# Optimization experiments

Hardware: AMD Instinct MI355X
Metric: run time of the kernel (lower is better)

Reference implementation:

```python
import jax, jax.numpy as jnp
import numpy as np

IOU_THRESH = 0.5
NEG_POS_RATIO = 3
VAR0, VAR1 = 0.1, 0.2  # BoxCoder variances


def box_iou(a, b):
    # a: [G,4] xyxy, b: [P,4] xyxy -> [G,P]
    lt = jnp.maximum(a[:, None, :2], b[None, :, :2])
    rb = jnp.minimum(a[:, None, 2:], b[None, :, 2:])
    wh = jnp.clip(rb - lt, 0.0)
    inter = wh[..., 0] * wh[..., 1]
    area_a = (a[:, 2] - a[:, 0]) * (a[:, 3] - a[:, 1])
    area_b = (b[:, 2] - b[:, 0]) * (b[:, 3] - b[:, 1])
    return inter / (area_a[:, None] + area_b[None, :] - inter)


def xywha_to_xyxy(p):
    c, wh = p[:, :2], p[:, 2:]
    return jnp.concatenate([c - wh * 0.5, c + wh * 0.5], axis=-1)


def assign_targets(gt_boxes, gt_labels, priors_xyxy):
    # gt_boxes [G,4], gt_labels [G], priors_xyxy [P,4]
    iou = box_iou(gt_boxes, priors_xyxy)            # [G,P]
    matched_vals = iou.max(axis=0)                  # [P]
    matches = iou.argmax(axis=0)                    # [P]
    best_prior = iou.argmax(axis=1)                 # [G] best prior per target
    G = gt_boxes.shape[0]
    matches = matches.at[best_prior].set(jnp.arange(G))
    matched_vals = matched_vals.at[best_prior].set(2.0)
    labels = jnp.where(matched_vals < IOU_THRESH, 0, gt_labels[matches])  # [P]
    boxes = gt_boxes[matches]                       # [P,4]
    return boxes, labels


def encode(boxes_xyxy, priors_xywha):
    # SSD center-form encoding with variances
    ctr = (boxes_xyxy[:, :2] + boxes_xyxy[:, 2:]) * 0.5
    wh = boxes_xyxy[:, 2:] - boxes_xyxy[:, :2]
    g_c = (ctr - priors_xywha[:, :2]) / (VAR0 * priors_xywha[:, 2:])
    g_wh = jnp.log(wh / priors_xywha[:, 2:]) / VAR1
    return jnp.concatenate([g_c, g_wh], axis=-1)


def hard_negative_mask(bg_loss, labels):
    # bg_loss [B,P]: -log_softmax(logits)[...,0]; keep all positives and
    # top-(ratio*num_pos) hardest negatives per image.
    pos = labels > 0
    num_neg = pos.sum(axis=1, keepdims=True) * NEG_POS_RATIO
    loss = jnp.where(pos, -jnp.inf, bg_loss)
    order = jnp.argsort(-loss, axis=1)
    rank = jnp.argsort(order, axis=1)
    return pos | (rank < num_neg)


def reference(priors, class_logits, box_regression, gt_boxes, gt_labels):
    priors_xyxy = xywha_to_xyxy(priors)
    boxes, labels = jax.vmap(assign_targets, in_axes=(0, 0, None))(
        gt_boxes, gt_labels, priors_xyxy)            # [B,P,4], [B,P]
    regression_targets = jax.vmap(encode, in_axes=(0, None))(boxes, priors)

    logp = jax.nn.log_softmax(class_logits, axis=-1)  # [B,P,C]
    bg_loss = jax.lax.stop_gradient(-logp[..., 0])
    mask = hard_negative_mask(bg_loss, labels)        # [B,P] bool

    # masked cross-entropy, reduction='sum'
    ce = -jnp.take_along_axis(logp, labels[..., None], axis=-1)[..., 0]
    loss_classifier = jnp.sum(jnp.where(mask, ce, 0.0))

    # masked smooth-L1 (beta=1), reduction='sum' over positives
    pos = labels > 0
    d = jnp.abs(box_regression - regression_targets)
    sl1 = jnp.where(d < 1.0, 0.5 * d * d, d - 0.5)
    loss_box_reg = jnp.sum(jnp.where(pos[..., None], sl1, 0.0))

    num_pos = jnp.sum(pos).astype(class_logits.dtype)
    return loss_box_reg / num_pos, loss_classifier / num_pos


def setup_inputs() -> dict:
    key = jax.random.key(0)
    ks = jax.random.split(key, 8)
    B, P, C, G = 64, 8732, 81, 16
    # priors: xywha in [0,1] with small positive wh
    p_c = jax.random.uniform(ks[0], (P, 2), jnp.float32, 0.05, 0.95)
    p_wh = jax.random.uniform(ks[1], (P, 2), jnp.float32, 0.02, 0.25)
    priors = jnp.concatenate([p_c, p_wh], axis=-1)
    class_logits = jax.random.normal(ks[2], (B, P, C), jnp.float32)
    box_regression = jax.random.normal(ks[3], (B, P, 4), jnp.float32)
    # gt boxes: valid xyxy in [0,1] with positive size
    g_c = jax.random.uniform(ks[4], (B, G, 2), jnp.float32, 0.2, 0.8)
    g_wh = jax.random.uniform(ks[5], (B, G, 2), jnp.float32, 0.05, 0.3)
    gt_boxes = jnp.concatenate([g_c - g_wh * 0.5, g_c + g_wh * 0.5], axis=-1)
    gt_labels = jax.random.randint(ks[6], (B, G), 1, C, jnp.int32)
    return {"priors": priors, "class_logits": class_logits,
            "box_regression": box_regression, "gt_boxes": gt_boxes,
            "gt_labels": gt_labels}
```

## Files before the change

kernel.cpp:

```cpp
#include <hip/hip_runtime.h>
#include <cfloat>

#define GT 16
#define NCLS 81
#define TPB 256
#define MAXP 8732
#define TROWS 64
#define WF4 324
#define TF4 (TROWS*NCLS/4)

__device__ __forceinline__ float smoothl1(float d){
  float a = fabsf(d);
  return a < 1.0f ? 0.5f*a*a : a - 0.5f;
}

__global__ __launch_bounds__(TPB) void assign1(
    const float* __restrict__ priors,
    const float* __restrict__ gt_boxes,
    long long* __restrict__ best,
    float* __restrict__ mvv,
    unsigned char* __restrict__ mmatch,
    float* __restrict__ ce_pos, float* __restrict__ sl1_sum,
    int* __restrict__ num_pos, float* __restrict__ out,
    int P)
{
  const int b = blockIdx.x >> 3, chunk = blockIdx.x & 7;
  const int CH = (P + 7) >> 3;
  const int p0 = chunk*CH, p1 = min(p0 + CH, P);
  const int tid = threadIdx.x, wave = tid >> 6, lane = tid & 63;
  if (chunk == 0 && tid == 0){ ce_pos[b] = 0.0f; sl1_sum[b] = 0.0f; num_pos[b] = 0; }
  if (blockIdx.x == 0 && tid < 2) out[tid] = 0.0f;
  __shared__ float gx0[GT], gy0[GT], gx1[GT], gy1[GT], ga[GT];
  __shared__ float redv[4*GT]; __shared__ int redi[4*GT];
  if (tid < GT){
    const float4 gb = ((const float4*)gt_boxes)[b*GT + tid];
    gx0[tid]=gb.x; gy0[tid]=gb.y; gx1[tid]=gb.z; gy1[tid]=gb.w;
    ga[tid] = (gb.z-gb.x)*(gb.w-gb.y);
  }
  __syncthreads();
  float bv[GT]; int bi[GT];
  #pragma unroll
  for (int g=0; g<GT; ++g){ bv[g] = -1.0f; bi[g] = 0x7fffffff; }
  for (int p = p0 + tid; p < p1; p += TPB){
    const float4 pr = ((const float4*)priors)[p];
    const float px0 = pr.x - pr.z*0.5f, py0 = pr.y - pr.w*0.5f;
    const float px1 = pr.x + pr.z*0.5f, py1 = pr.y + pr.w*0.5f;
    const float pa = (px1-px0)*(py1-py0);
    float mv = -1.0f; int mi = 0;
    #pragma unroll
    for (int g=0; g<GT; ++g){
      const float w = fmaxf(fminf(gx1[g],px1) - fmaxf(gx0[g],px0), 0.0f);
      const float h = fmaxf(fminf(gy1[g],py1) - fmaxf(gy0[g],py0), 0.0f);
      const float inter = w*h;
      const float iou = inter / (ga[g] + pa - inter);
      if (iou > mv){ mv = iou; mi = g; }
      if (iou > bv[g]){ bv[g] = iou; bi[g] = p; }
    }
    mvv[(long long)b*P + p] = mv;
    mmatch[(long long)b*P + p] = (unsigned char)mi;
  }
  #pragma unroll
  for (int g=0; g<GT; ++g){
    float v = bv[g]; int i = bi[g];
    for (int off=32; off>0; off>>=1){
      const float ov = __shfl_down(v, off);
      const int   oi = __shfl_down(i, off);
      if (ov > v || (ov == v && oi < i)){ v = ov; i = oi; }
    }
    if (lane == 0){ redv[wave*GT+g] = v; redi[wave*GT+g] = i; }
  }
  __syncthreads();
  if (tid < GT){
    float v = redv[tid]; int i = redi[tid];
    for (int w=1; w<4; ++w){
      const float ov = redv[w*GT+tid]; const int oi = redi[w*GT+tid];
      if (ov > v || (ov == v && oi < i)){ v = ov; i = oi; }
    }
    const long long pk =
      ((long long)(unsigned long long)__float_as_uint(v) << 32)
      | (long long)(0xFFFFFFFFu - (unsigned)i);
    atomicMax(&best[b*GT + tid], pk);
  }
}

__global__ __launch_bounds__(TPB) void assign2(
    const float* __restrict__ priors,
    const float* __restrict__ gt_boxes,
    const int*   __restrict__ gt_labels,
    const float* __restrict__ box_reg,
    const long long* __restrict__ best,
    const float* __restrict__ mvv,
    const unsigned char* __restrict__ mmatch,
    int*   __restrict__ labels_out,
    float* __restrict__ sl1_sum,
    int*   __restrict__ num_pos,
    int P)
{
  const int b = blockIdx.x >> 3, chunk = blockIdx.x & 7;
  const int CH = (P + 7) >> 3;
  const int p0 = chunk*CH, p1 = min(p0 + CH, P);
  const int tid = threadIdx.x, wave = tid >> 6, lane = tid & 63;
  __shared__ float gx0[GT], gy0[GT], gx1[GT], gy1[GT];
  __shared__ int glab[GT], bp[GT];
  __shared__ float rs[4]; __shared__ int rc[4];
  if (tid < GT){
    const float4 gb = ((const float4*)gt_boxes)[b*GT + tid];
    gx0[tid]=gb.x; gy0[tid]=gb.y; gx1[tid]=gb.z; gy1[tid]=gb.w;
    glab[tid] = gt_labels[b*GT + tid];
    bp[tid] = (int)(0xFFFFFFFFu - (unsigned)((unsigned long long)best[b*GT + tid] & 0xFFFFFFFFull));
  }
  __syncthreads();
  float sl1 = 0.0f; int cnt = 0;
  for (int p = p0 + tid; p < p1; p += TPB){
    float mv = mvv[(long long)b*P + p];
    int g = mmatch[(long long)b*P + p];
    #pragma unroll
    for (int g2=0; g2<GT; ++g2) if (bp[g2] == p){ mv = 2.0f; g = g2; }
    int lab = 0;
    if (mv >= 0.5f){
      lab = glab[g]; cnt++;
      const float4 pr = ((const float4*)priors)[p];
      const float ctrx = (gx0[g]+gx1[g])*0.5f, ctry = (gy0[g]+gy1[g])*0.5f;
      const float wx = gx1[g]-gx0[g], wy = gy1[g]-gy0[g];
      const float tx = (ctrx - pr.x) / (0.1f*pr.z);
      const float ty = (ctry - pr.y) / (0.1f*pr.w);
      const float tw = __logf(wx/pr.z) / 0.2f;
      const float th = __logf(wy/pr.w) / 0.2f;
      const float4 br = ((const float4*)box_reg)[(long long)b*P + p];
      sl1 += smoothl1(br.x - tx) + smoothl1(br.y - ty)
           + smoothl1(br.z - tw) + smoothl1(br.w - th);
    }
    labels_out[(long long)b*P + p] = lab;
  }
  float v = sl1; int c = cnt;
  for (int off=32; off>0; off>>=1){ v += __shfl_down(v, off); c += __shfl_down(c, off); }
  if (lane == 0){ rs[wave] = v; rc[wave] = c; }
  __syncthreads();
  if (tid == 0){
    atomicAdd(&sl1_sum[b], rs[0]+rs[1]+rs[2]+rs[3]);
    atomicAdd(&num_pos[b], rc[0]+rc[1]+rc[2]+rc[3]);
  }
}

__global__ __launch_bounds__(TPB) void lse_pipe(
    const float* __restrict__ logits,
    const int*   __restrict__ labels,
    float* __restrict__ bg,
    float* __restrict__ ce_pos,
    int P, int NT)
{
  __shared__ float s[TROWS*NCLS];
  const int tid = threadIdx.x;
  const int wave = tid >> 6, lane = tid & 63;
  const int rl = lane >> 2, q = lane & 3;
  const int c0 = q ? (1+20*q) : 0;
  const int c1 = 21 + 20*q;
  const int G = gridDim.x;
  int t = blockIdx.x;
  if (t >= NT) return;

  float4 r0,r1,r2,r3,r4,r5; int labc = 0;
  {
    const float4* src = (const float4*)logits + (long long)t*TF4 + wave*WF4;
    r0 = src[lane]; r1 = src[lane+64]; r2 = src[lane+128];
    r3 = src[lane+192]; r4 = src[lane+256];
    if (lane < 4) r5 = src[lane+320];
    if (q == 0) labc = labels[t*TROWS + wave*16 + rl];
  }
  float4* sd = (float4*)(s) + wave*WF4;
  const float* x = s + wave*(WF4*4) + rl*NCLS;
  for (; t < NT; t += G){
    sd[lane] = r0; sd[lane+64] = r1; sd[lane+128] = r2;
    sd[lane+192] = r3; sd[lane+256] = r4;
    if (lane < 4) sd[lane+320] = r5;
    const int lab = labc;
    const int tn = t + G;
    if (tn < NT){
      const float4* src = (const float4*)logits + (long long)tn*TF4 + wave*WF4;
      r0 = src[lane]; r1 = src[lane+64]; r2 = src[lane+128];
      r3 = src[lane+192]; r4 = src[lane+256];
      if (lane < 4) r5 = src[lane+320];
      if (q == 0) labc = labels[tn*TROWS + wave*16 + rl];
    }
    float sum = 0.0f;
    for (int c = c0; c < c1; ++c) sum += __expf(x[c]);
    sum += __shfl_xor(sum, 1);
    sum += __shfl_xor(sum, 2);
    if (q == 0){
      const int row = t*TROWS + wave*16 + rl;
      const float lse = __logf(sum);
      float bgv;
      if (lab > 0){
        const int b = row / P;
        const float xl = x[lab];
        atomicAdd(&ce_pos[b], lse - xl);
        bgv = 0.0f;
      } else {
        bgv = fmaxf(lse - x[0], 0.0f);
      }
      bg[row] = bgv;
    }
  }
}

__global__ __launch_bounds__(TPB) void topk_kernel(
    const float* __restrict__ bg,
    const int*   __restrict__ num_pos,
    const float* __restrict__ sl1_sum,
    const float* __restrict__ ce_pos,
    float* __restrict__ out,
    int P, int B)
{
  const int b = blockIdx.x;
  const int tid = threadIdx.x;
  const int wave = tid >> 6, lane = tid & 63;
  const int rep = tid & 15;
  __shared__ float sv[MAXP];
  __shared__ unsigned cntR[16][257];
  __shared__ unsigned s_wc[4];
  __shared__ float    s_wf[4];
  __shared__ unsigned s_prefix;
  __shared__ int s_krem, s_chosen, s_newk;

  {
    const float4* srcp = (const float4*)(bg + (long long)b * P);
    float4* dst = (float4*)sv;
    for (int j = tid; j < P/4; j += TPB) dst[j] = srcp[j];
  }
  if (tid == 0){
    const int k = 3*num_pos[b];
    s_krem = k < P ? k : P-1;
    s_prefix = 0u;
  }
  __syncthreads();

  for (int level=0; level<4; ++level){
    const int shift = 24 - 8*level;
    for (int i = tid; i < 16*257; i += TPB) ((unsigned*)cntR)[i] = 0u;
    __syncthreads();
    const unsigned pref = s_prefix;
    const int k = s_krem;
    for (int j = tid; j < P/4; j += TPB){
      const float4 f4 = ((const float4*)sv)[j];
      #pragma unroll
      for (int e=0; e<4; ++e){
        const unsigned key = __float_as_uint((&f4.x)[e]);
        const bool ok = (level == 0) || ((key >> (shift+8)) == pref);
        if (ok) atomicAdd(&cntR[rep][(key >> shift) & 255u], 1u);
      }
    }
    __syncthreads();
    const int rb = 255 - tid;
    unsigned c = 0;
    #pragma unroll
    for (int r=0; r<16; ++r) c += cntR[r][rb];
    unsigned cv = c;
    #pragma unroll
    for (int off=1; off<64; off<<=1){
      const unsigned oc = __shfl_up(cv, off);
      if (lane >= off) cv += oc;
    }
    if (lane == 63) s_wc[wave] = cv;
    __syncthreads();
    unsigned addc = 0;
    for (int w=0; w<4; ++w) if (w < wave) addc += s_wc[w];
    const unsigned S = cv - c + addc;
    if ((int)S <= k && k < (int)(S + c)){
      s_chosen = rb; s_newk = k - (int)S;
    }
    __syncthreads();
    if (tid == 0){
      s_krem = s_newk;
      s_prefix = (pref << 8) | (unsigned)s_chosen;
    }
    __syncthreads();
  }
  const unsigned T = s_prefix;
  float acc = 0.0f;
  for (int j = tid; j < P/4; j += TPB){
    const float4 f4 = ((const float4*)sv)[j];
    #pragma unroll
    for (int e=0; e<4; ++e){
      const float f = (&f4.x)[e];
      if (__float_as_uint(f) > T) acc += f;
    }
  }
  for (int off=32; off>0; off>>=1) acc += __shfl_down(acc, off);
  if (lane == 0) s_wf[wave] = acc;
  __syncthreads();
  if (tid < 64){
    float n = 0.0f;
    for (int i = tid; i < B; i += 64) n += (float)num_pos[i];
    for (int off=32; off>0; off>>=1) n += __shfl_down(n, off);
    if (tid == 0){
      const float N = n;
      const float cls = s_wf[0]+s_wf[1]+s_wf[2]+s_wf[3]
                      + (float)s_krem * __uint_as_float(T);
      atomicAdd(&out[0], sl1_sum[b] / N);
      atomicAdd(&out[1], (ce_pos[b] + cls) / N);
    }
  }
}

extern "C" void kernel_launch(void* const* d_in, const int* in_sizes, int n_in,
                              void* d_out, int out_size, void* d_ws, size_t ws_size,
                              hipStream_t stream) {
  const float* priors = (const float*)d_in[0];
  const float* logits = (const float*)d_in[1];
  const float* boxreg = (const float*)d_in[2];
  const float* gtb    = (const float*)d_in[3];
  const int*   gtl    = (const int*)d_in[4];
  const int P = in_sizes[0] / 4;
  const int B = in_sizes[4] / GT;
  const long long BP = (long long)B * P;

  char* ws = (char*)d_ws;
  int*   labels = (int*)ws;
  float* bgmv   = (float*)(ws + BP*4);
  unsigned char* mmatch = (unsigned char*)(ws + BP*8);
  char* tail = ws + BP*9;
  long long* best = (long long*)tail;
  float* sl1_s  = (float*)(tail + (long long)B*GT*8);
  int*   npos   = (int*)  (tail + (long long)B*GT*8 + 256);
  float* ce_pos = (float*)(tail + (long long)B*GT*8 + 512);

  assign1<<<B*8, TPB, 0, stream>>>(priors, gtb, best, bgmv, mmatch,
                                   ce_pos, sl1_s, npos, (float*)d_out, P);
  assign2<<<B*8, TPB, 0, stream>>>(priors, gtb, gtl, boxreg, best, bgmv, mmatch,
                                   labels, sl1_s, npos, P);
  const int NT = (int)(BP / TROWS);
  const int G = 1792;
  lse_pipe<<<G, TPB, 0, stream>>>(logits, labels, bgmv, ce_pos, P, NT);
  topk_kernel<<<B, TPB, 0, stream>>>(bgmv, npos, sl1_s, ce_pos, (float*)d_out, P, B);
}
```

Measured before the change: 339.1 us.

## Fuse target assignment and box loss into the log-softmax streaming kernel

The assign1/assign2 pair is replaced by one best-prior-per-target kernel (one 1024-thread block per image) and a fused kernel. The fused kernel recomputes per-prior IoU matching, labels and smooth-L1 inside the logits streaming loop. This drops the intermediate matched-value, match-index and label buffers and one launch. In exchange it adds redundant IoU work and per-positive global atomics to sl1_sum/num_pos inside the bandwidth-bound kernel.

Measured after the change: 367.9 us. 1.08x slower.

```diff
diff --git a/kernel.cpp b/kernel.cpp
--- a/kernel.cpp
+++ b/kernel.cpp
@@ -4,6 +4,7 @@
 #define GT 16
 #define NCLS 81
 #define TPB 256
+#define BPT 1024
 #define MAXP 8732
 #define TROWS 64
 #define WF4 324
@@ -14,24 +15,19 @@
   return a < 1.0f ? 0.5f*a*a : a - 0.5f;
 }
 
-__global__ __launch_bounds__(TPB) void assign1(
+__global__ __launch_bounds__(BPT) void bestprior(
     const float* __restrict__ priors,
     const float* __restrict__ gt_boxes,
-    long long* __restrict__ best,
-    float* __restrict__ mvv,
-    unsigned char* __restrict__ mmatch,
+    int*   __restrict__ best,
     float* __restrict__ ce_pos, float* __restrict__ sl1_sum,
-    int* __restrict__ num_pos, float* __restrict__ out,
-    int P)
+    int* __restrict__ num_pos, float* __restrict__ out, int P)
 {
-  const int b = blockIdx.x >> 3, chunk = blockIdx.x & 7;
-  const int CH = (P + 7) >> 3;
-  const int p0 = chunk*CH, p1 = min(p0 + CH, P);
+  const int b = blockIdx.x;
   const int tid = threadIdx.x, wave = tid >> 6, lane = tid & 63;
-  if (chunk == 0 && tid == 0){ ce_pos[b] = 0.0f; sl1_sum[b] = 0.0f; num_pos[b] = 0; }
-  if (blockIdx.x == 0 && tid < 2) out[tid] = 0.0f;
   __shared__ float gx0[GT], gy0[GT], gx1[GT], gy1[GT], ga[GT];
-  __shared__ float redv[4*GT]; __shared__ int redi[4*GT];
+  __shared__ float redv[16*GT]; __shared__ int redi[16*GT];
+  if (tid == 0){ ce_pos[b] = 0.0f; sl1_sum[b] = 0.0f; num_pos[b] = 0; }
+  if (b == 0 && tid < 2) out[tid] = 0.0f;
   if (tid < GT){
     const float4 gb = ((const float4*)gt_boxes)[b*GT + tid];
     gx0[tid]=gb.x; gy0[tid]=gb.y; gx1[tid]=gb.z; gy1[tid]=gb.w;
@@ -41,23 +37,19 @@
   float bv[GT]; int bi[GT];
   #pragma unroll
   for (int g=0; g<GT; ++g){ bv[g] = -1.0f; bi[g] = 0x7fffffff; }
-  for (int p = p0 + tid; p < p1; p += TPB){
+  for (int p = tid; p < P; p += BPT){
     const float4 pr = ((const float4*)priors)[p];
     const float px0 = pr.x - pr.z*0.5f, py0 = pr.y - pr.w*0.5f;
     const float px1 = pr.x + pr.z*0.5f, py1 = pr.y + pr.w*0.5f;
     const float pa = (px1-px0)*(py1-py0);
-    float mv = -1.0f; int mi = 0;
     #pragma unroll
     for (int g=0; g<GT; ++g){
       const float w = fmaxf(fminf(gx1[g],px1) - fmaxf(gx0[g],px0), 0.0f);
       const float h = fmaxf(fminf(gy1[g],py1) - fmaxf(gy0[g],py0), 0.0f);
       const float inter = w*h;
       const float iou = inter / (ga[g] + pa - inter);
-      if (iou > mv){ mv = iou; mi = g; }
       if (iou > bv[g]){ bv[g] = iou; bi[g] = p; }
     }
-    mvv[(long long)b*P + p] = mv;
-    mmatch[(long long)b*P + p] = (unsigned char)mi;
   }
   #pragma unroll
   for (int g=0; g<GT; ++g){
@@ -72,81 +64,25 @@
   __syncthreads();
   if (tid < GT){
     float v = redv[tid]; int i = redi[tid];
-    for (int w=1; w<4; ++w){
+    for (int w=1; w<16; ++w){
       const float ov = redv[w*GT+tid]; const int oi = redi[w*GT+tid];
       if (ov > v || (ov == v && oi < i)){ v = ov; i = oi; }
     }
-    const long long pk =
-      ((long long)(unsigned long long)__float_as_uint(v) << 32)
-      | (long long)(0xFFFFFFFFu - (unsigned)i);
-    atomicMax(&best[b*GT + tid], pk);
-  }
-}
-
-__global__ __launch_bounds__(TPB) void assign2(
+    best[b*GT + tid] = i;
+  }
+}
+
+__global__ __launch_bounds__(TPB) void fused_lse(
     const float* __restrict__ priors,
     const float* __restrict__ gt_boxes,
     const int*   __restrict__ gt_labels,
     const float* __restrict__ box_reg,
-    const long long* __restrict__ best,
-    const float* __restrict__ mvv,
-    const unsigned char* __restrict__ mmatch,
-    int*   __restrict__ labels_out,
+    const int*   __restrict__ best,
+    const float* __restrict__ logits,
+    float* __restrict__ bg,
+    float* __restrict__ ce_pos,
     float* __restrict__ sl1_sum,
     int*   __restrict__ num_pos,
-    int P)
-{
-  const int b = blockIdx.x >> 3, chunk = blockIdx.x & 7;
-  const int CH = (P + 7) >> 3;
-  const int p0 = chunk*CH, p1 = min(p0 + CH, P);
-  const int tid = threadIdx.x, wave = tid >> 6, lane = tid & 63;
-  __shared__ float gx0[GT], gy0[GT], gx1[GT], gy1[GT];
-  __shared__ int glab[GT], bp[GT];
-  __shared__ float rs[4]; __shared__ int rc[4];
-  if (tid < GT){
-    const float4 gb = ((const float4*)gt_boxes)[b*GT + tid];
-    gx0[tid]=gb.x; gy0[tid]=gb.y; gx1[tid]=gb.z; gy1[tid]=gb.w;
-    glab[tid] = gt_labels[b*GT + tid];
-    bp[tid] = (int)(0xFFFFFFFFu - (unsigned)((unsigned long long)best[b*GT + tid] & 0xFFFFFFFFull));
-  }
-  __syncthreads();
-  float sl1 = 0.0f; int cnt = 0;
-  for (int p = p0 + tid; p < p1; p += TPB){
-    float mv = mvv[(long long)b*P + p];
-    int g = mmatch[(long long)b*P + p];
-    #pragma unroll
-    for (int g2=0; g2<GT; ++g2) if (bp[g2] == p){ mv = 2.0f; g = g2; }
-    int lab = 0;
-    if (mv >= 0.5f){
-      lab = glab[g]; cnt++;
-      const float4 pr = ((const float4*)priors)[p];
-      const float ctrx = (gx0[g]+gx1[g])*0.5f, ctry = (gy0[g]+gy1[g])*0.5f;
-      const float wx = gx1[g]-gx0[g], wy = gy1[g]-gy0[g];
-      const float tx = (ctrx - pr.x) / (0.1f*pr.z);
-      const float ty = (ctry - pr.y) / (0.1f*pr.w);
-      const float tw = __logf(wx/pr.z) / 0.2f;
-      const float th = __logf(wy/pr.w) / 0.2f;
-      const float4 br = ((const float4*)box_reg)[(long long)b*P + p];
-      sl1 += smoothl1(br.x - tx) + smoothl1(br.y - ty)
-           + smoothl1(br.z - tw) + smoothl1(br.w - th);
-    }
-    labels_out[(long long)b*P + p] = lab;
-  }
-  float v = sl1; int c = cnt;
-  for (int off=32; off>0; off>>=1){ v += __shfl_down(v, off); c += __shfl_down(c, off); }
-  if (lane == 0){ rs[wave] = v; rc[wave] = c; }
-  __syncthreads();
-  if (tid == 0){
-    atomicAdd(&sl1_sum[b], rs[0]+rs[1]+rs[2]+rs[3]);
-    atomicAdd(&num_pos[b], rc[0]+rc[1]+rc[2]+rc[3]);
-  }
-}
-
-__global__ __launch_bounds__(TPB) void lse_pipe(
-    const float* __restrict__ logits,
-    const int*   __restrict__ labels,
-    float* __restrict__ bg,
-    float* __restrict__ ce_pos,
     int P, int NT)
 {
   __shared__ float s[TROWS*NCLS];
@@ -159,13 +95,12 @@
   int t = blockIdx.x;
   if (t >= NT) return;
 
-  float4 r0,r1,r2,r3,r4,r5; int labc = 0;
+  float4 r0,r1,r2,r3,r4,r5;
   {
     const float4* src = (const float4*)logits + (long long)t*TF4 + wave*WF4;
     r0 = src[lane]; r1 = src[lane+64]; r2 = src[lane+128];
     r3 = src[lane+192]; r4 = src[lane+256];
     if (lane < 4) r5 = src[lane+320];
-    if (q == 0) labc = labels[t*TROWS + wave*16 + rl];
   }
   float4* sd = (float4*)(s) + wave*WF4;
   const float* x = s + wave*(WF4*4) + rl*NCLS;
@@ -173,27 +108,66 @@
     sd[lane] = r0; sd[lane+64] = r1; sd[lane+128] = r2;
     sd[lane+192] = r3; sd[lane+256] = r4;
     if (lane < 4) sd[lane+320] = r5;
-    const int lab = labc;
     const int tn = t + G;
     if (tn < NT){
       const float4* src = (const float4*)logits + (long long)tn*TF4 + wave*WF4;
       r0 = src[lane]; r1 = src[lane+64]; r2 = src[lane+128];
       r3 = src[lane+192]; r4 = src[lane+256];
       if (lane < 4) r5 = src[lane+320];
-      if (q == 0) labc = labels[tn*TROWS + wave*16 + rl];
-    }
+    }
+
+    const int row = t*TROWS + wave*16 + rl;
+    const int b = row / P;
+    const int p = row - b*P;
+    int lab = 0;
+    if (q == 0){
+      const float4 pr = ((const float4*)priors)[p];
+      const float px0 = pr.x - pr.z*0.5f, py0 = pr.y - pr.w*0.5f;
+      const float px1 = pr.x + pr.z*0.5f, py1 = pr.y + pr.w*0.5f;
+      const float pa = (px1-px0)*(py1-py0);
+      const float4* gtb4 = (const float4*)gt_boxes + b*GT;
+      float mv = -1.0f; int mi = 0;
+      #pragma unroll
+      for (int g=0; g<GT; ++g){
+        const float4 gb = gtb4[g];
+        const float w = fmaxf(fminf(gb.z,px1) - fmaxf(gb.x,px0), 0.0f);
+        const float h = fmaxf(fminf(gb.w,py1) - fmaxf(gb.y,py0), 0.0f);
+        const float inter = w*h;
+        const float garea = (gb.z-gb.x)*(gb.w-gb.y);
+        const float iou = inter / (garea + pa - inter);
+        if (iou > mv){ mv = iou; mi = g; }
+      }
+      const int* bpp = best + b*GT;
+      #pragma unroll
+      for (int g2=0; g2<GT; ++g2){
+        if (bpp[g2] == p){ mv = 2.0f; mi = g2; }
+      }
+      if (mv >= 0.5f){
+        lab = gt_labels[b*GT + mi];
+        const float4 gb = gtb4[mi];
+        const float ctrx = (gb.x+gb.z)*0.5f, ctry = (gb.y+gb.w)*0.5f;
+        const float wx = gb.z-gb.x, wy = gb.w-gb.y;
+        const float tx = (ctrx - pr.x) / (0.1f*pr.z);
+        const float ty = (ctry - pr.y) / (0.1f*pr.w);
+        const float tw = __logf(wx/pr.z) / 0.2f;
+        const float th = __logf(wy/pr.w) / 0.2f;
+        const float4 br = ((const float4*)box_reg)[(long long)row];
+        const float s1 = smoothl1(br.x - tx) + smoothl1(br.y - ty)
+                       + smoothl1(br.z - tw) + smoothl1(br.w - th);
+        atomicAdd(&sl1_sum[b], s1);
+        atomicAdd(&num_pos[b], 1);
+      }
+    }
+
     float sum = 0.0f;
     for (int c = c0; c < c1; ++c) sum += __expf(x[c]);
     sum += __shfl_xor(sum, 1);
     sum += __shfl_xor(sum, 2);
     if (q == 0){
-      const int row = t*TROWS + wave*16 + rl;
       const float lse = __logf(sum);
       float bgv;
       if (lab > 0){
-        const int b = row / P;
-        const float xl = x[lab];
-        atomicAdd(&ce_pos[b], lse - xl);
+        atomicAdd(&ce_pos[b], lse - x[lab]);
         bgv = 0.0f;
       } else {
         bgv = fmaxf(lse - x[0], 0.0f);
@@ -315,21 +289,17 @@
   const long long BP = (long long)B * P;
 
   char* ws = (char*)d_ws;
-  int*   labels = (int*)ws;
-  float* bgmv   = (float*)(ws + BP*4);
-  unsigned char* mmatch = (unsigned char*)(ws + BP*8);
-  char* tail = ws + BP*9;
-  long long* best = (long long*)tail;
-  float* sl1_s  = (float*)(tail + (long long)B*GT*8);
-  int*   npos   = (int*)  (tail + (long long)B*GT*8 + 256);
-  float* ce_pos = (float*)(tail + (long long)B*GT*8 + 512);
-
-  assign1<<<B*8, TPB, 0, stream>>>(priors, gtb, best, bgmv, mmatch,
-                                   ce_pos, sl1_s, npos, (float*)d_out, P);
-  assign2<<<B*8, TPB, 0, stream>>>(priors, gtb, gtl, boxreg, best, bgmv, mmatch,
-                                   labels, sl1_s, npos, P);
+  float* bgv  = (float*)ws;
+  int*   best = (int*)(ws + BP*4);
+  float* sl1_s= (float*)(ws + BP*4 + 4096);
+  int*   npos = (int*)  (ws + BP*4 + 4352);
+  float* cep  = (float*)(ws + BP*4 + 4608);
+
+  bestprior<<<B, BPT, 0, stream>>>(priors, gtb, best, cep, sl1_s, npos,
+                                   (float*)d_out, P);
   const int NT = (int)(BP / TROWS);
   const int G = 1792;
-  lse_pipe<<<G, TPB, 0, stream>>>(logits, labels, bgmv, ce_pos, P, NT);
-  topk_kernel<<<B, TPB, 0, stream>>>(bgmv, npos, sl1_s, ce_pos, (float*)d_out, P, B);
-}
+  fused_lse<<<G, TPB, 0, stream>>>(priors, gtb, gtl, boxreg, best, logits,
+                                   bgv, cep, sl1_s, npos, P, NT);
+  topk_kernel<<<B, TPB, 0, stream>>>(bgv, npos, sl1_s, cep, (float*)d_out, P, B);
+}
```
